# Optimization experiments

Measured on AMD Instinct MI355X. Metric: run time of the kernel, lower is better.

Reference implementation:

```python
import jax, jax.numpy as jnp
import numpy as np

NU = 1.0  # degrees of freedom of the Student-t / Tsallis softmax


def setup_inputs() -> dict:
    key = jax.random.key(0)
    k1, k2, k3, k4 = jax.random.split(key, 4)
    B, Nx, Nh, Ny = 8192, 2048, 512, 1024
    x = jax.random.normal(k1, (B, Nx), dtype=jnp.float32)
    W_fc = jax.random.normal(k2, (Nh, Nx), dtype=jnp.float32) * (1.0 / np.sqrt(Nx))
    b_fc = jax.random.normal(k3, (Nh,), dtype=jnp.float32) * 0.01
    W_q = jax.random.normal(k4, (Ny, Nh), dtype=jnp.float32) * (1.0 / np.sqrt(Nh))
    return {"x": x, "W_fc": W_fc, "b_fc": b_fc, "W_q": W_q}


def reference(x, W_fc, b_fc, W_q):
    # x: [B, Nx] -> relu -> Linear(Nx, Nh) -> relu
    h = jax.nn.relu(jax.nn.relu(x) @ W_fc.T + b_fc)  # [B, Nh]
    # Quadratic layer: squared Euclidean distance to each class prototype.
    # ||h - w_j||^2 = ||h||^2 - 2 h.w_j + ||w_j||^2  (avoids [B, Ny, Nh] tensor)
    d = (jnp.sum(h * h, axis=-1, keepdims=True)
         - 2.0 * (h @ W_q.T)
         + jnp.sum(W_q * W_q, axis=-1))  # [B, Ny]
    d = jnp.maximum(d, 0.0)  # guard tiny negatives from fp cancellation
    # LogTSoftmax: p_j \propto (1 + d_j/nu)^{-(nu+1)/2}
    t = (-(NU + 1.0) / 2.0) * jnp.log1p(d / NU)  # [B, Ny]
    return t - jax.scipy.special.logsumexp(t, axis=-1, keepdims=True)
```

## Files before the change

kernel.cpp:

```cpp
#include <hip/hip_runtime.h>
#include <stdint.h>
#include <stddef.h>

#define B_ROWS 8192
#define NX 2048
#define NH 512
#define NY 1024

#define X_ELEMS (B_ROWS * NX)
#define EW_ELEMS (X_ELEMS + NH * NX)
#define EW_BLOCKS (EW_ELEMS / (8 * 256))
#define WQ_BLOCKS (NY / 4)

typedef __attribute__((ext_vector_type(8))) short bf16x8;
typedef __attribute__((ext_vector_type(4))) float f32x4;

static __device__ __forceinline__ unsigned short f2bf(float f) {
    union { float f; unsigned int u; } c; c.f = f;
    unsigned int r = 0x7FFFu + ((c.u >> 16) & 1u);
    return (unsigned short)((c.u + r) >> 16);
}

static __device__ __forceinline__ void glld16(const void* g, void* l) {
    __builtin_amdgcn_global_load_lds(
        (const __attribute__((address_space(1))) unsigned int*)g,
        (__attribute__((address_space(3))) unsigned int*)l, 16, 0, 0);
}

__global__ __launch_bounds__(256) void prep_kernel(const float* __restrict__ x,
                                                   const float* __restrict__ wfc,
                                                   const float* __restrict__ wq,
                                                   unsigned short* __restrict__ xb,
                                                   unsigned short* __restrict__ wfcb,
                                                   unsigned short* __restrict__ wqb,
                                                   float* __restrict__ wqsq,
                                                   float* __restrict__ hsq) {
    const int bid = blockIdx.x;
    const int tid = threadIdx.x;
    if (bid < EW_BLOCKS) {
        size_t idx = ((size_t)bid * 256 + tid) * 8;
        if (idx < (size_t)X_ELEMS) {
            float4 a = *(const float4*)&x[idx];
            float4 b = *(const float4*)&x[idx + 4];
            bf16x8 o;
            o[0] = (short)f2bf(fmaxf(a.x, 0.f)); o[1] = (short)f2bf(fmaxf(a.y, 0.f));
            o[2] = (short)f2bf(fmaxf(a.z, 0.f)); o[3] = (short)f2bf(fmaxf(a.w, 0.f));
            o[4] = (short)f2bf(fmaxf(b.x, 0.f)); o[5] = (short)f2bf(fmaxf(b.y, 0.f));
            o[6] = (short)f2bf(fmaxf(b.z, 0.f)); o[7] = (short)f2bf(fmaxf(b.w, 0.f));
            *(bf16x8*)&xb[idx] = o;
        } else {
            size_t off = idx - X_ELEMS;
            float4 a = *(const float4*)&wfc[off];
            float4 b = *(const float4*)&wfc[off + 4];
            bf16x8 o;
            o[0] = (short)f2bf(a.x); o[1] = (short)f2bf(a.y);
            o[2] = (short)f2bf(a.z); o[3] = (short)f2bf(a.w);
            o[4] = (short)f2bf(b.x); o[5] = (short)f2bf(b.y);
            o[6] = (short)f2bf(b.z); o[7] = (short)f2bf(b.w);
            *(bf16x8*)&wfcb[off] = o;
        }
    } else {
        const int b2 = bid - EW_BLOCKS;
        const int lane = tid & 63;
        const int row = b2 * 4 + (tid >> 6);
        const float* p = wq + (size_t)row * NH + lane * 8;
        float4 a = *(const float4*)p;
        float4 b = *(const float4*)(p + 4);
        bf16x8 o;
        o[0] = (short)f2bf(a.x); o[1] = (short)f2bf(a.y);
        o[2] = (short)f2bf(a.z); o[3] = (short)f2bf(a.w);
        o[4] = (short)f2bf(b.x); o[5] = (short)f2bf(b.y);
        o[6] = (short)f2bf(b.z); o[7] = (short)f2bf(b.w);
        *(bf16x8*)&wqb[(size_t)row * NH + lane * 8] = o;
        float s = a.x*a.x + a.y*a.y + a.z*a.z + a.w*a.w
                + b.x*b.x + b.y*b.y + b.z*b.z + b.w*b.w;
        #pragma unroll
        for (int off = 32; off > 0; off >>= 1) s += __shfl_xor(s, off);
        if (lane == 0) wqsq[row] = s;
        if (tid < 32) hsq[b2 * 32 + tid] = 0.0f;
    }
}

__global__ __launch_bounds__(512, 4) void gemm1_kernel(const unsigned short* __restrict__ xb,
                                                       const unsigned short* __restrict__ wfcb,
                                                       const float* __restrict__ b_fc,
                                                       unsigned short* __restrict__ hb,
                                                       float* __restrict__ hsq) {
    __shared__ unsigned char smem[24576];
    unsigned char* AsB = smem;
    unsigned char* BsB = smem + 16384;

    const int tid = threadIdx.x;
    const int lane = tid & 63;
    const int wave = tid >> 6;
    const int wm = wave & 3;
    const int wn = wave >> 2;
    const int quad = lane >> 4;
    const int r = lane & 15;

    const int bid = blockIdx.x;
    const int c_ = bid & 7, q_ = bid >> 3;
    const int n0 = (q_ & 7) * 64;
    const int m0 = ((c_ << 3) | (q_ >> 3)) * 128;

    f32x4 acc[2][2];
    #pragma unroll
    for (int i = 0; i < 2; ++i)
        #pragma unroll
        for (int j = 0; j < 2; ++j) acc[i][j] = (f32x4)(0.0f);

    const int lrow = lane >> 2;
    const int gch = (lane & 3) ^ ((lrow >> 1) & 3);
    const int fsw = (quad ^ ((r >> 1) & 3)) * 16;

    const char* asrc = (const char*)xb + (size_t)(m0 + wave * 16 + lrow) * (NX * 2) + gch * 16;
    const char* bsrc = (const char*)wfcb + (size_t)(n0 + (wave & 3) * 16 + lrow) * (NX * 2) + gch * 16;

    auto stage = [&](int buf, int k0) {
        glld16(asrc + (size_t)k0 * 2, AsB + buf * 8192 + wave * 1024);
        if (wave < 4)
            glld16(bsrc + (size_t)k0 * 2, BsB + buf * 4096 + wave * 1024);
    };

    stage(0, 0);
    asm volatile("s_waitcnt vmcnt(0)" ::: "memory");
    __builtin_amdgcn_s_barrier();
    __builtin_amdgcn_sched_barrier(0);

    #pragma unroll 1
    for (int it = 0; it < NX / 32; ++it) {
        if (it + 1 < NX / 32) stage((it + 1) & 1, it * 32 + 32);
        __builtin_amdgcn_sched_barrier(0);
        const unsigned char* ab = AsB + (it & 1) * 8192;
        const unsigned char* bb = BsB + (it & 1) * 4096;
        bf16x8 af[2], bfv[2];
        #pragma unroll
        for (int i = 0; i < 2; ++i)
            af[i] = *(const bf16x8*)(ab + (wm * 32 + i * 16 + r) * 64 + fsw);
        #pragma unroll
        for (int j = 0; j < 2; ++j)
            bfv[j] = *(const bf16x8*)(bb + (wn * 32 + j * 16 + r) * 64 + fsw);
        #pragma unroll
        for (int i = 0; i < 2; ++i)
            #pragma unroll
            for (int j = 0; j < 2; ++j)
                acc[i][j] = __builtin_amdgcn_mfma_f32_16x16x32_bf16(af[i], bfv[j], acc[i][j], 0, 0, 0);
        __builtin_amdgcn_sched_barrier(0);
        asm volatile("s_waitcnt vmcnt(0)" ::: "memory");
        __builtin_amdgcn_s_barrier();
        __builtin_amdgcn_sched_barrier(0);
    }

    float p[2][4];
    #pragma unroll
    for (int i = 0; i < 2; ++i)
        #pragma unroll
        for (int rr = 0; rr < 4; ++rr) p[i][rr] = 0.0f;

    #pragma unroll
    for (int j = 0; j < 2; ++j) {
        int col = n0 + wn * 32 + j * 16 + r;
        float bias = b_fc[col];
        #pragma unroll
        for (int i = 0; i < 2; ++i) {
            int rowb = m0 + wm * 32 + i * 16 + quad * 4;
            #pragma unroll
            for (int rr = 0; rr < 4; ++rr) {
                float v = fmaxf(acc[i][j][rr] + bias, 0.0f);
                hb[(size_t)(rowb + rr) * NH + col] = f2bf(v);
                p[i][rr] += v * v;
            }
        }
    }
    #pragma unroll
    for (int mask = 1; mask < 16; mask <<= 1)
        #pragma unroll
        for (int i = 0; i < 2; ++i)
            #pragma unroll
            for (int rr = 0; rr < 4; ++rr)
                p[i][rr] += __shfl_xor(p[i][rr], mask);
    if (r == 0) {
        #pragma unroll
        for (int i = 0; i < 2; ++i)
            #pragma unroll
            for (int rr = 0; rr < 4; ++rr)
                atomicAdd(&hsq[m0 + wm * 32 + i * 16 + quad * 4 + rr], p[i][rr]);
    }
}

__global__ __launch_bounds__(512, 2) void gemm2_kernel(const unsigned short* __restrict__ hb,
                                                       const unsigned short* __restrict__ wqb,
                                                       const float* __restrict__ hsq,
                                                       const float* __restrict__ wqsq,
                                                       float* __restrict__ out) {
    __shared__ unsigned char smem[163840];
    char* As = (char*)smem;
    char* Bs = (char*)smem + 32768;

    const int tid = threadIdx.x;
    const int lane = tid & 63;
    const int wave = tid >> 6;
    const int quad = lane >> 4;
    const int r = lane & 15;
    const int m0 = blockIdx.x * 32;

    f32x4 acc[2][8];
    #pragma unroll
    for (int i = 0; i < 2; ++i)
        #pragma unroll
        for (int j = 0; j < 8; ++j) acc[i][j] = (f32x4)(0.0f);

    const int lrow = lane >> 2;
    const int gch = (lane & 3) ^ ((lrow >> 1) & 3);
    const int fsw = (quad ^ ((r >> 1) & 3)) * 16;

    const char* bsrc = (const char*)wqb + (size_t)(wave * 128 + lrow) * (NH * 2) + gch * 16;

    auto stageB = [&](int buf, int k0) {
        #pragma unroll
        for (int c = 0; c < 8; ++c)
            glld16(bsrc + (size_t)(c * 16 * NH + k0) * 2,
                   Bs + buf * 65536 + (wave * 128 + c * 16) * 64);
    };

    #pragma unroll
    for (int g = 0; g < 4; ++g) {
        int slab = 2 * wave + (g >> 1);
        int half = g & 1;
        glld16((const char*)hb + (size_t)(m0 + half * 16 + lrow) * (NH * 2) + slab * 64 + gch * 16,
               As + slab * 2048 + half * 1024);
    }
    stageB(0, 0);
    asm volatile("s_waitcnt vmcnt(0)" ::: "memory");
    __builtin_amdgcn_s_barrier();
    __builtin_amdgcn_sched_barrier(0);

    #pragma unroll 1
    for (int it = 0; it < NH / 32; ++it) {
        if (it + 1 < NH / 32) stageB((it + 1) & 1, it * 32 + 32);
        __builtin_amdgcn_sched_barrier(0);
        const char* ab = As + it * 2048;
        const char* bb = Bs + (it & 1) * 65536;
        bf16x8 af[2];
        #pragma unroll
        for (int i = 0; i < 2; ++i)
            af[i] = *(const bf16x8*)(ab + (i * 16 + r) * 64 + fsw);
        #pragma unroll
        for (int jh = 0; jh < 2; ++jh) {
            bf16x8 bfv[4];
            #pragma unroll
            for (int j = 0; j < 4; ++j)
                bfv[j] = *(const bf16x8*)(bb + (wave * 128 + jh * 64 + j * 16 + r) * 64 + fsw);
            #pragma unroll
            for (int i = 0; i < 2; ++i)
                #pragma unroll
                for (int j = 0; j < 4; ++j)
                    acc[i][jh * 4 + j] = __builtin_amdgcn_mfma_f32_16x16x32_bf16(af[i], bfv[j], acc[i][jh * 4 + j], 0, 0, 0);
        }
        __builtin_amdgcn_sched_barrier(0);
        asm volatile("s_waitcnt vmcnt(0)" ::: "memory");
        __builtin_amdgcn_s_barrier();
        __builtin_amdgcn_sched_barrier(0);
    }

    float hs_[2][4];
    #pragma unroll
    for (int i = 0; i < 2; ++i)
        #pragma unroll
        for (int rr = 0; rr < 4; ++rr)
            hs_[i][rr] = hsq[m0 + i * 16 + quad * 4 + rr];

    float srow[2][4];
    #pragma unroll
    for (int i = 0; i < 2; ++i)
        #pragma unroll
        for (int rr = 0; rr < 4; ++rr) srow[i][rr] = 0.0f;

    #pragma unroll
    for (int j = 0; j < 8; ++j) {
        float wqv = wqsq[wave * 128 + j * 16 + r];
        #pragma unroll
        for (int i = 0; i < 2; ++i) {
            #pragma unroll
            for (int rr = 0; rr < 4; ++rr) {
                float d = hs_[i][rr] - 2.0f * acc[i][j][rr] + wqv;
                d = fmaxf(d, 0.0f);
                float onepd = 1.0f + d;
                srow[i][rr] += __builtin_amdgcn_rcpf(onepd);
                acc[i][j][rr] = -__logf(onepd);
            }
        }
    }
    #pragma unroll
    for (int mask = 1; mask < 16; mask <<= 1)
        #pragma unroll
        for (int i = 0; i < 2; ++i)
            #pragma unroll
            for (int rr = 0; rr < 4; ++rr)
                srow[i][rr] += __shfl_xor(srow[i][rr], mask);

    float* smemF = (float*)smem;
    if (r == 0) {
        #pragma unroll
        for (int i = 0; i < 2; ++i)
            #pragma unroll
            for (int rr = 0; rr < 4; ++rr)
                smemF[wave * 32 + i * 16 + quad * 4 + rr] = srow[i][rr];
    }
    __syncthreads();
    if (tid < 32) {
        float S = 0.0f;
        #pragma unroll
        for (int w = 0; w < 8; ++w) S += smemF[w * 32 + tid];
        smemF[256 + tid] = __logf(S);
    }
    __syncthreads();

    #pragma unroll
    for (int i = 0; i < 2; ++i) {
        #pragma unroll
        for (int rr = 0; rr < 4; ++rr) {
            float l = smemF[256 + i * 16 + quad * 4 + rr];
            size_t rowoff = (size_t)(m0 + i * 16 + quad * 4 + rr) * NY + wave * 128 + r;
            #pragma unroll
            for (int j = 0; j < 8; ++j)
                out[rowoff + j * 16] = acc[i][j][rr] - l;
        }
    }
}

extern "C" void kernel_launch(void* const* d_in, const int* in_sizes, int n_in,
                              void* d_out, int out_size, void* d_ws, size_t ws_size,
                              hipStream_t stream) {
    const float* x    = (const float*)d_in[0];
    const float* W_fc = (const float*)d_in[1];
    const float* b_fc = (const float*)d_in[2];
    const float* W_q  = (const float*)d_in[3];
    float* out = (float*)d_out;

    char* ws = (char*)d_ws;
    unsigned short* xb   = (unsigned short*)(ws);
    unsigned short* wfcb = (unsigned short*)(ws + 33554432);
    unsigned short* wqb  = (unsigned short*)(ws + 35651584);
    float*          wqsq = (float*)(ws + 36700160);
    unsigned short* hb   = (unsigned short*)(ws + 36704256);
    float*          hsq  = (float*)(ws + 45092864);

    prep_kernel<<<EW_BLOCKS + WQ_BLOCKS, 256, 0, stream>>>(x, W_fc, W_q, xb, wfcb, wqb, wqsq, hsq);
    gemm1_kernel<<<512, 512, 0, stream>>>(xb, wfcb, b_fc, hb, hsq);
    gemm2_kernel<<<B_ROWS / 32, 512, 0, stream>>>(hb, wqb, hsq, wqsq, out);
}
```

Measured before the change: 174.3 us.

## Triple-buffer GEMM1 with 64-wide K tiles and relax GEMM2 per-iteration sync

GEMM1 moves from a double-buffered, 32-wide K loop to a triple-buffered, 64-wide K loop. It uses a new XOR swizzle over 128-byte LDS rows and partial vmcnt waits, so only one barrier is needed per iteration and loads run two stages ahead. GEMM2 uses partial vmcnt waits and drops its trailing per-iteration barrier, relying on each wave owning its own B slab. The main costs are that GEMM1's LDS footprint grows to 72KB, which can lower resident blocks per CU, and that removing GEMM2's barrier depends on per-wave buffer ownership for correctness.

```diff
diff --git a/kernel.cpp b/kernel.cpp
--- a/kernel.cpp
+++ b/kernel.cpp
@@ -86,9 +86,9 @@
                                                        const float* __restrict__ b_fc,
                                                        unsigned short* __restrict__ hb,
                                                        float* __restrict__ hsq) {
-    __shared__ unsigned char smem[24576];
+    __shared__ unsigned char smem[73728];
     unsigned char* AsB = smem;
-    unsigned char* BsB = smem + 16384;
+    unsigned char* BsB = smem + 49152;
 
     const int tid = threadIdx.x;
     const int lane = tid & 63;
@@ -97,6 +97,7 @@
     const int wn = wave >> 2;
     const int quad = lane >> 4;
     const int r = lane & 15;
+    const int rx = r & 7;
 
     const int bid = blockIdx.x;
     const int c_ = bid & 7, q_ = bid >> 3;
@@ -109,46 +110,52 @@
         #pragma unroll
         for (int j = 0; j < 2; ++j) acc[i][j] = (f32x4)(0.0f);
 
-    const int lrow = lane >> 2;
-    const int gch = (lane & 3) ^ ((lrow >> 1) & 3);
-    const int fsw = (quad ^ ((r >> 1) & 3)) * 16;
-
-    const char* asrc = (const char*)xb + (size_t)(m0 + wave * 16 + lrow) * (NX * 2) + gch * 16;
-    const char* bsrc = (const char*)wfcb + (size_t)(n0 + (wave & 3) * 16 + lrow) * (NX * 2) + gch * 16;
-
-    auto stage = [&](int buf, int k0) {
-        glld16(asrc + (size_t)k0 * 2, AsB + buf * 8192 + wave * 1024);
-        if (wave < 4)
-            glld16(bsrc + (size_t)k0 * 2, BsB + buf * 4096 + wave * 1024);
+    const int lrow8 = lane >> 3;
+    const int gch8 = (lane & 7) ^ lrow8;
+
+    const char* a0 = (const char*)xb + (size_t)(m0 + wave * 16 + lrow8) * (NX * 2) + gch8 * 16;
+    const char* a1 = a0 + (size_t)8 * (NX * 2);
+    const char* bsrc = (const char*)wfcb + (size_t)(n0 + wave * 8 + lrow8) * (NX * 2) + gch8 * 16;
+
+    auto stage = [&](int bi, int k0) {
+        glld16(a0 + (size_t)k0 * 2, AsB + bi * 16384 + (wave * 16) * 128);
+        glld16(a1 + (size_t)k0 * 2, AsB + bi * 16384 + (wave * 16 + 8) * 128);
+        glld16(bsrc + (size_t)k0 * 2, BsB + bi * 8192 + (wave * 8) * 128);
     };
 
     stage(0, 0);
-    asm volatile("s_waitcnt vmcnt(0)" ::: "memory");
-    __builtin_amdgcn_s_barrier();
-    __builtin_amdgcn_sched_barrier(0);
-
+    stage(1, 64);
+
+    int cb = 0, sb = 2;
     #pragma unroll 1
-    for (int it = 0; it < NX / 32; ++it) {
-        if (it + 1 < NX / 32) stage((it + 1) & 1, it * 32 + 32);
-        __builtin_amdgcn_sched_barrier(0);
-        const unsigned char* ab = AsB + (it & 1) * 8192;
-        const unsigned char* bb = BsB + (it & 1) * 4096;
-        bf16x8 af[2], bfv[2];
-        #pragma unroll
-        for (int i = 0; i < 2; ++i)
-            af[i] = *(const bf16x8*)(ab + (wm * 32 + i * 16 + r) * 64 + fsw);
-        #pragma unroll
-        for (int j = 0; j < 2; ++j)
-            bfv[j] = *(const bf16x8*)(bb + (wn * 32 + j * 16 + r) * 64 + fsw);
-        #pragma unroll
-        for (int i = 0; i < 2; ++i)
+    for (int it = 0; it < NX / 64; ++it) {
+        if (it == NX / 64 - 1) { asm volatile("s_waitcnt vmcnt(0)" ::: "memory"); }
+        else                   { asm volatile("s_waitcnt vmcnt(3)" ::: "memory"); }
+        __builtin_amdgcn_sched_barrier(0);
+        __builtin_amdgcn_s_barrier();
+        __builtin_amdgcn_sched_barrier(0);
+        if (it + 2 < NX / 64) stage(sb, it * 64 + 128);
+        __builtin_amdgcn_sched_barrier(0);
+        const unsigned char* ab = AsB + cb * 16384;
+        const unsigned char* bb = BsB + cb * 8192;
+        #pragma unroll
+        for (int s = 0; s < 2; ++s) {
+            const int ch = ((s * 4 + quad) ^ rx) * 16;
+            bf16x8 af[2], bfv[2];
+            #pragma unroll
+            for (int i = 0; i < 2; ++i)
+                af[i] = *(const bf16x8*)(ab + (wm * 32 + i * 16 + r) * 128 + ch);
             #pragma unroll
             for (int j = 0; j < 2; ++j)
-                acc[i][j] = __builtin_amdgcn_mfma_f32_16x16x32_bf16(af[i], bfv[j], acc[i][j], 0, 0, 0);
-        __builtin_amdgcn_sched_barrier(0);
-        asm volatile("s_waitcnt vmcnt(0)" ::: "memory");
-        __builtin_amdgcn_s_barrier();
-        __builtin_amdgcn_sched_barrier(0);
+                bfv[j] = *(const bf16x8*)(bb + (wn * 32 + j * 16 + r) * 128 + ch);
+            #pragma unroll
+            for (int i = 0; i < 2; ++i)
+                #pragma unroll
+                for (int j = 0; j < 2; ++j)
+                    acc[i][j] = __builtin_amdgcn_mfma_f32_16x16x32_bf16(af[i], bfv[j], acc[i][j], 0, 0, 0);
+        }
+        cb = (cb == 2) ? 0 : cb + 1;
+        sb = (sb == 2) ? 0 : sb + 1;
     }
 
     float p[2][4];
@@ -231,13 +238,17 @@
                As + slab * 2048 + half * 1024);
     }
     stageB(0, 0);
-    asm volatile("s_waitcnt vmcnt(0)" ::: "memory");
+    asm volatile("s_waitcnt vmcnt(8)" ::: "memory");
+    __builtin_amdgcn_sched_barrier(0);
     __builtin_amdgcn_s_barrier();
     __builtin_amdgcn_sched_barrier(0);
 
     #pragma unroll 1
     for (int it = 0; it < NH / 32; ++it) {
         if (it + 1 < NH / 32) stageB((it + 1) & 1, it * 32 + 32);
+        __builtin_amdgcn_sched_barrier(0);
+        if (it == NH / 32 - 1) { asm volatile("s_waitcnt vmcnt(0)" ::: "memory"); }
+        else                   { asm volatile("s_waitcnt vmcnt(8)" ::: "memory"); }
         __builtin_amdgcn_sched_barrier(0);
         const char* ab = As + it * 2048;
         const char* bb = Bs + (it & 1) * 65536;
@@ -257,10 +268,6 @@
                 for (int j = 0; j < 4; ++j)
                     acc[i][jh * 4 + j] = __builtin_amdgcn_mfma_f32_16x16x32_bf16(af[i], bfv[j], acc[i][jh * 4 + j], 0, 0, 0);
         }
-        __builtin_amdgcn_sched_barrier(0);
-        asm volatile("s_waitcnt vmcnt(0)" ::: "memory");
-        __builtin_amdgcn_s_barrier();
-        __builtin_amdgcn_sched_barrier(0);
     }
 
     float hs_[2][4];
@@ -300,6 +307,7 @@
                 srow[i][rr] += __shfl_xor(srow[i][rr], mask);
 
     float* smemF = (float*)smem;
+    __syncthreads();
     if (r == 0) {
         #pragma unroll
         for (int i = 0; i < 2; ++i)
```

New measurement: 165.2 us. 5.2% less time.
